# Performance work log

Measured on AMD Instinct MI355X. Metric: run time of the kernel, lower is better.

Reference implementation:

```python
import jax, jax.numpy as jnp
import numpy as np

SC = 30.0
M = 0.5
EPS = 1e-12  # F.normalize default eps


def _l2norm(x, axis):
    n = jnp.sqrt(jnp.sum(x * x, axis=axis, keepdims=True))
    return x / jnp.maximum(n, EPS)


def setup_inputs() -> dict:
    key = jax.random.key(0)
    k1, k2, k3, k4, k5 = jax.random.split(key, 5)
    n, in_f, out_f, books, words = 1024, 2048, 4096, 8, 256
    lw = in_f // books  # len_word = 256
    # xavier_uniform-ish scale for params
    w_lim = np.sqrt(6.0 / (out_f + lw))
    m_lim = np.sqrt(6.0 / (lw + words))
    return {
        "input": jax.random.normal(k1, (n, in_f), dtype=jnp.float32),
        "label": jax.random.randint(k2, (n,), 0, out_f, dtype=jnp.int64),
        "weight": jax.random.uniform(k3, (books, out_f, lw), jnp.float32, -w_lim, w_lim),
        "mlp": jax.random.uniform(k4, (books, lw, words), jnp.float32, -m_lim, m_lim),
        "codebooks": jax.random.normal(k5, (books, lw, words), dtype=jnp.float32),
    }


def reference(input, label, weight, mlp, codebooks):
    n, in_f = input.shape
    books, out_f, lw = weight.shape
    # split input into per-book chunks: [books, n, lw]
    x = input.reshape(n, books, lw).transpose(1, 0, 2)
    wn = _l2norm(weight, axis=2)               # [books, out_f, lw]
    xn = _l2norm(x, axis=2)                    # [books, n, lw]
    cos_xw = jnp.clip(jnp.einsum('bnd,bod->bno', xn, wn), -1.0, 1.0)  # [books,n,out_f]
    # per-book soft codeword assignment
    xc_soft = jax.nn.softmax(jnp.einsum('bnd,bdw->bnw', x, mlp), axis=2)  # [books,n,words]
    # soft-quantized features s_m: codebooks @ xc_soft^T -> [books, lw, n] -> [books, n, lw]
    s = jnp.einsum('bdw,bnw->bnd', codebooks, xc_soft)
    sn = _l2norm(s, axis=2)
    cos_sw = jnp.clip(jnp.einsum('bnd,bod->bno', sn, wn), -1.0, 1.0)
    # margin one-hot combine: oh*(cos - m) + (1-oh)*cos == cos - oh*m
    oh = jax.nn.one_hot(label, out_f, dtype=cos_xw.dtype)[None]  # [1, n, out_f]
    out1 = SC * (cos_xw - oh * M)
    out2 = SC * (cos_sw - oh * M)
    return (out1.transpose(1, 0, 2), out2.transpose(1, 0, 2), xc_soft.transpose(1, 0, 2))
```

## Files before the change

kernel.cpp:

```cpp
#include <hip/hip_runtime.h>

typedef __attribute__((ext_vector_type(8))) short short8;
typedef __attribute__((ext_vector_type(4))) float f32x4;
typedef __attribute__((ext_vector_type(8))) unsigned short u16x8;

#define BOOKS 8
#define NSAMP 1024
#define OUTF  4096
#define KDIM  256
#define OUT2_OFF 33554432ull
#define OUT3_OFF 67108864ull

__device__ __forceinline__ unsigned short f2bf(float f) {
  unsigned int u = __float_as_uint(f);
  u += 0x7fffu + ((u >> 16) & 1u);
  return (unsigned short)(u >> 16);
}
__device__ __forceinline__ float b2f(unsigned short u) {
  return __uint_as_float((unsigned)u << 16);
}

__device__ __forceinline__ float wave_sum(float v) {
  #pragma unroll
  for (int off = 32; off; off >>= 1) v += __shfl_xor(v, off, 64);
  return v;
}
__device__ __forceinline__ float qsum(float v) {
  #pragma unroll
  for (int off = 1; off < 16; off <<= 1) v += __shfl_xor(v, off, 64);
  return v;
}
__device__ __forceinline__ float qmax(float v) {
  #pragma unroll
  for (int off = 1; off < 16; off <<= 1) v = fmaxf(v, __shfl_xor(v, off, 64));
  return v;
}

__device__ __forceinline__ void gll16(const void* g, void* l) {
  __builtin_amdgcn_global_load_lds((const __attribute__((address_space(1))) void*)g,
                                   (__attribute__((address_space(3))) void*)l,
                                   16, 0, 0);
}

__global__ __launch_bounds__(256) void prep_kernel(const float* __restrict__ input,
                                                   const float* __restrict__ weight,
                                                   const float* __restrict__ mlp,
                                                   const float* __restrict__ cb,
                                                   unsigned short* __restrict__ wn,
                                                   unsigned short* __restrict__ Xb,
                                                   unsigned short* __restrict__ An,
                                                   unsigned short* __restrict__ mlpT,
                                                   unsigned short* __restrict__ cbb) {
  __shared__ float lt[64][65];
  const int blk = blockIdx.x;
  const int tid = threadIdx.x;

  if (blk < 8192) {
    int row  = blk * 4 + (tid >> 6);
    int lane = tid & 63;
    float4 v = ((const float4*)(weight + (size_t)row * KDIM))[lane];
    float ss = wave_sum(v.x*v.x + v.y*v.y + v.z*v.z + v.w*v.w);
    float inv = 1.f / fmaxf(sqrtf(ss), 1e-12f);
    ushort4 o;
    o.x = f2bf(v.x*inv); o.y = f2bf(v.y*inv); o.z = f2bf(v.z*inv); o.w = f2bf(v.w*inv);
    *(ushort4*)(wn + (size_t)row * KDIM + lane * 4) = o;
  } else if (blk < 10240) {
    int id = (blk - 8192) * 4 + (tid >> 6);
    int b = id >> 10, i = id & 1023;
    int lane = tid & 63;
    float4 v = ((const float4*)(input + (size_t)i * 2048 + b * 256))[lane];
    float ss = wave_sum(v.x*v.x + v.y*v.y + v.z*v.z + v.w*v.w);
    float inv = 1.f / fmaxf(sqrtf(ss), 1e-12f);
    ushort4 r;
    r.x = f2bf(v.x); r.y = f2bf(v.y); r.z = f2bf(v.z); r.w = f2bf(v.w);
    *(ushort4*)(Xb + (size_t)id * KDIM + lane * 4) = r;
    ushort4 n;
    n.x = f2bf(v.x*inv); n.y = f2bf(v.y*inv); n.z = f2bf(v.z*inv); n.w = f2bf(v.w*inv);
    *(ushort4*)(An + ((size_t)b * 2048 + i) * KDIM + lane * 4) = n;
  } else {
    int t = blk - 10240;
    int b = t >> 4, tile = t & 15;
    int dt = (tile >> 2) * 64, wt = (tile & 3) * 64;
    int g  = tid >> 4;
    int l4 = (tid & 15) * 4;
    const float* mb = mlp + (size_t)b * 256 * 256;
    const float* cs = cb  + (size_t)b * 256 * 256;
    #pragma unroll
    for (int p = 0; p < 4; ++p) {
      int d = dt + p * 16 + g;
      float4 v = *(const float4*)(mb + (size_t)d * 256 + wt + l4);
      lt[p * 16 + g][l4 + 0] = v.x;
      lt[p * 16 + g][l4 + 1] = v.y;
      lt[p * 16 + g][l4 + 2] = v.z;
      lt[p * 16 + g][l4 + 3] = v.w;
      float4 c = *(const float4*)(cs + (size_t)d * 256 + wt + l4);
      ushort4 co;
      co.x = f2bf(c.x); co.y = f2bf(c.y); co.z = f2bf(c.z); co.w = f2bf(c.w);
      *(ushort4*)(cbb + ((size_t)(b * 256 + d)) * 256 + wt + l4) = co;
    }
    __syncthreads();
    #pragma unroll
    for (int p = 0; p < 4; ++p) {
      int w = wt + p * 16 + g;
      ushort4 o;
      o.x = f2bf(lt[l4 + 0][p * 16 + g]);
      o.y = f2bf(lt[l4 + 1][p * 16 + g]);
      o.z = f2bf(lt[l4 + 2][p * 16 + g]);
      o.w = f2bf(lt[l4 + 3][p * 16 + g]);
      *(ushort4*)(mlpT + ((size_t)(b * 256 + w)) * 256 + dt + l4) = o;
    }
  }
}

__global__ __launch_bounds__(256) void mid_kernel(const unsigned short* __restrict__ Xb,
                                                  const unsigned short* __restrict__ mlpT,
                                                  const unsigned short* __restrict__ cbb,
                                                  unsigned short* __restrict__ An,
                                                  float* __restrict__ out3) {
  __shared__ __align__(16) unsigned short lA[64 * 32];
  __shared__ __align__(16) unsigned short lB[256 * 32];
  __shared__ __align__(16) unsigned short lX[64 * 256];

  const int b  = blockIdx.x >> 4;
  const int m0 = (blockIdx.x & 15) * 64;
  const int tid  = threadIdx.x;
  const int wv   = tid >> 6;
  const int lane = tid & 63;
  const int r16  = lane & 15;
  const int q    = lane >> 4;

  const unsigned short* Ab = Xb   + ((size_t)b * NSAMP + m0) * KDIM;
  const unsigned short* Bm = mlpT + (size_t)b * 256 * KDIM;
  const unsigned short* Bc = cbb  + (size_t)b * 256 * KDIM;

  f32x4 acc[16];
  #pragma unroll
  for (int j = 0; j < 16; ++j) acc[j] = (f32x4){0.f, 0.f, 0.f, 0.f};

  for (int k0 = 0; k0 < KDIM; k0 += 32) {
    __syncthreads();
    { int row = tid >> 2, ko = (tid & 3) * 8;
      gll16(Ab + (size_t)row * KDIM + k0 + ko, &lA[tid * 8]); }
    #pragma unroll
    for (int c = 0; c < 4; ++c) {
      int idx = c * 256 + tid;
      int row = idx >> 2, ko = (idx & 3) * 8;
      gll16(Bm + (size_t)row * KDIM + k0 + ko, &lB[idx * 8]);
    }
    __syncthreads();
    short8 af = *(const short8*)(lA + (wv * 16 + r16) * 32 + q * 8);
    #pragma unroll
    for (int j = 0; j < 16; ++j) {
      short8 bf = *(const short8*)(lB + (j * 16 + r16) * 32 + q * 8);
      acc[j] = __builtin_amdgcn_mfma_f32_16x16x32_bf16(af, bf, acc[j], 0, 0, 0);
    }
  }

  #pragma unroll
  for (int r = 0; r < 4; ++r) {
    float mx = acc[0][r];
    #pragma unroll
    for (int j = 1; j < 16; ++j) mx = fmaxf(mx, acc[j][r]);
    mx = qmax(mx);
    float s = 0.f;
    #pragma unroll
    for (int j = 0; j < 16; ++j) { float e = __expf(acc[j][r] - mx); acc[j][r] = e; s += e; }
    s = qsum(s);
    float inv = 1.f / s;
    int row = wv * 16 + q * 4 + r;
    unsigned rb  = (unsigned)row * 512;
    unsigned msk = ((unsigned)(row & 7)) << 4;
    #pragma unroll
    for (int j = 0; j < 16; ++j) {
      unsigned byte = (rb + (unsigned)(j * 16 + r16) * 2) ^ msk;
      *(unsigned short*)((char*)lX + byte) = f2bf(acc[j][r] * inv);
    }
  }
  __syncthreads();

  #pragma unroll
  for (int p = 0; p < 8; ++p) {
    int chunk = p * 256 + tid;
    int row = chunk >> 5;
    int c8  = (chunk & 31) * 8;
    unsigned byte = ((unsigned)(row * 512 + c8 * 2)) ^ (((unsigned)(row & 7)) << 4);
    u16x8 v = *(const u16x8*)((char*)lX + byte);
    size_t o = ((size_t)(m0 + row) * 8 + b) * 256 + c8;
    f32x4 f0 = { b2f(v[0]), b2f(v[1]), b2f(v[2]), b2f(v[3]) };
    f32x4 f1 = { b2f(v[4]), b2f(v[5]), b2f(v[6]), b2f(v[7]) };
    __builtin_nontemporal_store(f0, (f32x4*)(out3 + o));
    __builtin_nontemporal_store(f1, (f32x4*)(out3 + o + 4));
  }

  #pragma unroll
  for (int j = 0; j < 16; ++j) acc[j] = (f32x4){0.f, 0.f, 0.f, 0.f};
  for (int k0 = 0; k0 < KDIM; k0 += 32) {
    __syncthreads();
    #pragma unroll
    for (int c = 0; c < 4; ++c) {
      int idx = c * 256 + tid;
      int row = idx >> 2, ko = (idx & 3) * 8;
      gll16(Bc + (size_t)row * KDIM + k0 + ko, &lB[idx * 8]);
    }
    __syncthreads();
    int arow = wv * 16 + r16;
    unsigned abyte = ((unsigned)(arow * 512 + (k0 + q * 8) * 2)) ^ (((unsigned)(arow & 7)) << 4);
    short8 af = *(const short8*)((char*)lX + abyte);
    #pragma unroll
    for (int j = 0; j < 16; ++j) {
      short8 bf = *(const short8*)(lB + (j * 16 + r16) * 32 + q * 8);
      acc[j] = __builtin_amdgcn_mfma_f32_16x16x32_bf16(af, bf, acc[j], 0, 0, 0);
    }
  }

  #pragma unroll
  for (int r = 0; r < 4; ++r) {
    float ss = 0.f;
    #pragma unroll
    for (int j = 0; j < 16; ++j) ss += acc[j][r] * acc[j][r];
    ss = qsum(ss);
    float iv = 1.f / fmaxf(sqrtf(ss), 1e-12f);
    int row = wv * 16 + q * 4 + r;
    unsigned rb  = (unsigned)row * 512;
    unsigned msk = ((unsigned)(row & 7)) << 4;
    #pragma unroll
    for (int j = 0; j < 16; ++j) {
      unsigned byte = (rb + (unsigned)(j * 16 + r16) * 2) ^ msk;
      *(unsigned short*)((char*)lX + byte) = f2bf(acc[j][r] * iv);
    }
  }
  __syncthreads();
  #pragma unroll
  for (int p = 0; p < 8; ++p) {
    int chunk = p * 256 + tid;
    int row = chunk >> 5;
    int c8  = (chunk & 31) * 8;
    unsigned byte = ((unsigned)(row * 512 + c8 * 2)) ^ (((unsigned)(row & 7)) << 4);
    u16x8 v = *(const u16x8*)((char*)lX + byte);
    *(u16x8*)(An + ((size_t)b * 2048 + 1024 + m0 + row) * KDIM + c8) = v;
  }
}

__global__ __launch_bounds__(256) void big_gemm_kernel(const unsigned short* __restrict__ A,
                                                       const unsigned short* __restrict__ B,
                                                       float* __restrict__ Cf,
                                                       const int* __restrict__ label) {
  __shared__ __align__(16) unsigned short lA[128 * 32];
  __shared__ __align__(16) unsigned short lB[128 * 32];

  const int b  = blockIdx.z;
  const int lin = blockIdx.x + (blockIdx.y << 5);
  const int wg  = ((lin & 7) << 6) + (lin >> 3);
  const int n0 = (wg & 31) * 128;
  const int m0 = (wg >> 5) * 128;
  const int tid  = threadIdx.x;
  const int wid  = tid >> 6;
  const int lane = tid & 63;
  const int wm = wid & 1, wn = wid >> 1;
  const int r16 = lane & 15;
  const int q   = lane >> 4;

  const unsigned short* Ab = A + (size_t)b * 2048 * KDIM;
  const unsigned short* Bb = B + (size_t)b * OUTF * KDIM;

  f32x4 acc[4][4];
  #pragma unroll
  for (int i = 0; i < 4; ++i)
    #pragma unroll
    for (int j = 0; j < 4; ++j) acc[i][j] = (f32x4){0.f, 0.f, 0.f, 0.f};

  for (int k0 = 0; k0 < KDIM; k0 += 32) {
    __syncthreads();
    #pragma unroll
    for (int c = 0; c < 2; ++c) {
      int idx = c * 256 + tid;
      int row = idx >> 2, ko = (idx & 3) * 8;
      gll16(Ab + (size_t)(m0 + row) * KDIM + k0 + ko, &lA[idx * 8]);
      gll16(Bb + (size_t)(n0 + row) * KDIM + k0 + ko, &lB[idx * 8]);
    }
    __syncthreads();

    short8 af[4], bfr[4];
    #pragma unroll
    for (int f = 0; f < 4; ++f) {
      af[f]  = *(const short8*)(lA + (wm * 64 + f * 16 + r16) * 32 + q * 8);
      bfr[f] = *(const short8*)(lB + (wn * 64 + f * 16 + r16) * 32 + q * 8);
    }
    #pragma unroll
    for (int i = 0; i < 4; ++i)
      #pragma unroll
      for (int j = 0; j < 4; ++j)
        acc[i][j] = __builtin_amdgcn_mfma_f32_16x16x32_bf16(af[i], bfr[j], acc[i][j], 0, 0, 0);
  }

  #pragma unroll
  for (int i = 0; i < 4; ++i) {
    int row0 = m0 + wm * 64 + i * 16 + q * 4;
    #pragma unroll
    for (int r = 0; r < 4; ++r) {
      int row = row0 + r;
      int gi  = row & 1023;
      int lb  = label[gi];
      size_t base = (size_t)(row >> 10) * OUT2_OFF + ((size_t)gi * 8 + b) * OUTF;
      #pragma unroll
      for (int j = 0; j < 4; ++j) {
        int col = n0 + wn * 64 + j * 16 + r16;
        float v = fminf(fmaxf(acc[i][j][r], -1.f), 1.f) * 30.f;
        if (col == lb) v -= 15.f;
        __builtin_nontemporal_store(v, &Cf[base + col]);
      }
    }
  }
}

extern "C" void kernel_launch(void* const* d_in, const int* in_sizes, int n_in,
                              void* d_out, int out_size, void* d_ws, size_t ws_size,
                              hipStream_t stream) {
  const float* input  = (const float*)d_in[0];
  const int*   label  = (const int*)d_in[1];
  const float* weight = (const float*)d_in[2];
  const float* mlp    = (const float*)d_in[3];
  const float* cb     = (const float*)d_in[4];
  float* out = (float*)d_out;

  unsigned short* wn = (unsigned short*)d_ws;
  unsigned short* An = wn + 8388608;

  unsigned short* Xb   = (unsigned short*)(out + OUT2_OFF);
  unsigned short* mlpT = Xb + 2097152;
  unsigned short* cbb  = mlpT + 524288;
  float*          out3 = out + OUT3_OFF;

  prep_kernel<<<dim3(10368), dim3(256), 0, stream>>>(input, weight, mlp, cb,
                                                     wn, Xb, An, mlpT, cbb);
  mid_kernel<<<dim3(128), dim3(256), 0, stream>>>(Xb, mlpT, cbb, An, out3);
  big_gemm_kernel<<<dim3(32, 16, 8), dim3(256), 0, stream>>>(An, wn, out, label);
}
```

Before: 373.7 us.

## Split mid_kernel across more blocks with cross-wave row reductions; drop GEMM block swizzle

mid_kernel now uses 256 blocks of 512 threads, each handling 32 rows instead of 64. The 256 output columns are split across four wave groups, so the softmax max/sum and the L2 norm are combined through shared-memory partials with extra barriers. The aim is better occupancy and more CU coverage for a kernel that previously launched only 128 blocks. Separately, the big GEMM drops its XCD-aware block-index swizzle in favour of a direct blockIdx mapping, which may change L2 locality.

```diff
diff --git a/kernel.cpp b/kernel.cpp
--- a/kernel.cpp
+++ b/kernel.cpp
@@ -112,20 +112,25 @@
   }
 }
 
-__global__ __launch_bounds__(256) void mid_kernel(const unsigned short* __restrict__ Xb,
+__global__ __launch_bounds__(512) void mid_kernel(const unsigned short* __restrict__ Xb,
                                                   const unsigned short* __restrict__ mlpT,
                                                   const unsigned short* __restrict__ cbb,
                                                   unsigned short* __restrict__ An,
                                                   float* __restrict__ out3) {
-  __shared__ __align__(16) unsigned short lA[64 * 32];
+  __shared__ __align__(16) unsigned short lA[32 * 32];
   __shared__ __align__(16) unsigned short lB[256 * 32];
-  __shared__ __align__(16) unsigned short lX[64 * 256];
-
-  const int b  = blockIdx.x >> 4;
-  const int m0 = (blockIdx.x & 15) * 64;
+  __shared__ __align__(16) unsigned short lX[32 * 256];
+  __shared__ float smx[32][4];
+  __shared__ float ssm[32][4];
+  __shared__ float sqs[32][4];
+
+  const int b  = blockIdx.x >> 5;
+  const int m0 = (blockIdx.x & 31) * 32;
   const int tid  = threadIdx.x;
-  const int wv   = tid >> 6;
+  const int wid  = tid >> 6;
   const int lane = tid & 63;
+  const int wm = wid & 1;
+  const int wj = wid >> 1;
   const int r16  = lane & 15;
   const int q    = lane >> 4;
 
@@ -133,54 +138,67 @@
   const unsigned short* Bm = mlpT + (size_t)b * 256 * KDIM;
   const unsigned short* Bc = cbb  + (size_t)b * 256 * KDIM;
 
-  f32x4 acc[16];
-  #pragma unroll
-  for (int j = 0; j < 16; ++j) acc[j] = (f32x4){0.f, 0.f, 0.f, 0.f};
+  f32x4 acc[4];
+  #pragma unroll
+  for (int j = 0; j < 4; ++j) acc[j] = (f32x4){0.f, 0.f, 0.f, 0.f};
 
   for (int k0 = 0; k0 < KDIM; k0 += 32) {
     __syncthreads();
-    { int row = tid >> 2, ko = (tid & 3) * 8;
-      gll16(Ab + (size_t)row * KDIM + k0 + ko, &lA[tid * 8]); }
-    #pragma unroll
-    for (int c = 0; c < 4; ++c) {
-      int idx = c * 256 + tid;
+    if (tid < 128) {
+      int row = tid >> 2, ko = (tid & 3) * 8;
+      gll16(Ab + (size_t)row * KDIM + k0 + ko, &lA[tid * 8]);
+    }
+    #pragma unroll
+    for (int c = 0; c < 2; ++c) {
+      int idx = c * 512 + tid;
       int row = idx >> 2, ko = (idx & 3) * 8;
       gll16(Bm + (size_t)row * KDIM + k0 + ko, &lB[idx * 8]);
     }
     __syncthreads();
-    short8 af = *(const short8*)(lA + (wv * 16 + r16) * 32 + q * 8);
-    #pragma unroll
-    for (int j = 0; j < 16; ++j) {
-      short8 bf = *(const short8*)(lB + (j * 16 + r16) * 32 + q * 8);
+    short8 af = *(const short8*)(lA + (wm * 16 + r16) * 32 + q * 8);
+    #pragma unroll
+    for (int j = 0; j < 4; ++j) {
+      short8 bf = *(const short8*)(lB + ((wj * 4 + j) * 16 + r16) * 32 + q * 8);
       acc[j] = __builtin_amdgcn_mfma_f32_16x16x32_bf16(af, bf, acc[j], 0, 0, 0);
     }
   }
 
   #pragma unroll
   for (int r = 0; r < 4; ++r) {
-    float mx = acc[0][r];
-    #pragma unroll
-    for (int j = 1; j < 16; ++j) mx = fmaxf(mx, acc[j][r]);
+    float mx = fmaxf(fmaxf(acc[0][r], acc[1][r]), fmaxf(acc[2][r], acc[3][r]));
     mx = qmax(mx);
+    int rt = wm * 16 + q * 4 + r;
+    if (r16 == 0) smx[rt][wj] = mx;
+  }
+  __syncthreads();
+  #pragma unroll
+  for (int r = 0; r < 4; ++r) {
+    int rt = wm * 16 + q * 4 + r;
+    float mx = fmaxf(fmaxf(smx[rt][0], smx[rt][1]), fmaxf(smx[rt][2], smx[rt][3]));
     float s = 0.f;
     #pragma unroll
-    for (int j = 0; j < 16; ++j) { float e = __expf(acc[j][r] - mx); acc[j][r] = e; s += e; }
+    for (int j = 0; j < 4; ++j) { float e = __expf(acc[j][r] - mx); acc[j][r] = e; s += e; }
     s = qsum(s);
-    float inv = 1.f / s;
-    int row = wv * 16 + q * 4 + r;
-    unsigned rb  = (unsigned)row * 512;
-    unsigned msk = ((unsigned)(row & 7)) << 4;
-    #pragma unroll
-    for (int j = 0; j < 16; ++j) {
-      unsigned byte = (rb + (unsigned)(j * 16 + r16) * 2) ^ msk;
+    if (r16 == 0) ssm[rt][wj] = s;
+  }
+  __syncthreads();
+  #pragma unroll
+  for (int r = 0; r < 4; ++r) {
+    int rt = wm * 16 + q * 4 + r;
+    float inv = 1.f / (ssm[rt][0] + ssm[rt][1] + ssm[rt][2] + ssm[rt][3]);
+    unsigned rb  = (unsigned)rt * 512;
+    unsigned msk = ((unsigned)(rt & 7)) << 4;
+    #pragma unroll
+    for (int j = 0; j < 4; ++j) {
+      unsigned byte = (rb + (unsigned)((wj * 4 + j) * 16 + r16) * 2) ^ msk;
       *(unsigned short*)((char*)lX + byte) = f2bf(acc[j][r] * inv);
     }
   }
   __syncthreads();
 
   #pragma unroll
-  for (int p = 0; p < 8; ++p) {
-    int chunk = p * 256 + tid;
+  for (int p = 0; p < 2; ++p) {
+    int chunk = p * 512 + tid;
     int row = chunk >> 5;
     int c8  = (chunk & 31) * 8;
     unsigned byte = ((unsigned)(row * 512 + c8 * 2)) ^ (((unsigned)(row & 7)) << 4);
@@ -193,22 +211,22 @@
   }
 
   #pragma unroll
-  for (int j = 0; j < 16; ++j) acc[j] = (f32x4){0.f, 0.f, 0.f, 0.f};
+  for (int j = 0; j < 4; ++j) acc[j] = (f32x4){0.f, 0.f, 0.f, 0.f};
   for (int k0 = 0; k0 < KDIM; k0 += 32) {
     __syncthreads();
     #pragma unroll
-    for (int c = 0; c < 4; ++c) {
-      int idx = c * 256 + tid;
+    for (int c = 0; c < 2; ++c) {
+      int idx = c * 512 + tid;
       int row = idx >> 2, ko = (idx & 3) * 8;
       gll16(Bc + (size_t)row * KDIM + k0 + ko, &lB[idx * 8]);
     }
     __syncthreads();
-    int arow = wv * 16 + r16;
+    int arow = wm * 16 + r16;
     unsigned abyte = ((unsigned)(arow * 512 + (k0 + q * 8) * 2)) ^ (((unsigned)(arow & 7)) << 4);
     short8 af = *(const short8*)((char*)lX + abyte);
     #pragma unroll
-    for (int j = 0; j < 16; ++j) {
-      short8 bf = *(const short8*)(lB + (j * 16 + r16) * 32 + q * 8);
+    for (int j = 0; j < 4; ++j) {
+      short8 bf = *(const short8*)(lB + ((wj * 4 + j) * 16 + r16) * 32 + q * 8);
       acc[j] = __builtin_amdgcn_mfma_f32_16x16x32_bf16(af, bf, acc[j], 0, 0, 0);
     }
   }
@@ -217,22 +235,29 @@
   for (int r = 0; r < 4; ++r) {
     float ss = 0.f;
     #pragma unroll
-    for (int j = 0; j < 16; ++j) ss += acc[j][r] * acc[j][r];
+    for (int j = 0; j < 4; ++j) ss += acc[j][r] * acc[j][r];
     ss = qsum(ss);
-    float iv = 1.f / fmaxf(sqrtf(ss), 1e-12f);
-    int row = wv * 16 + q * 4 + r;
-    unsigned rb  = (unsigned)row * 512;
-    unsigned msk = ((unsigned)(row & 7)) << 4;
-    #pragma unroll
-    for (int j = 0; j < 16; ++j) {
-      unsigned byte = (rb + (unsigned)(j * 16 + r16) * 2) ^ msk;
+    int rt = wm * 16 + q * 4 + r;
+    if (r16 == 0) sqs[rt][wj] = ss;
+  }
+  __syncthreads();
+  #pragma unroll
+  for (int r = 0; r < 4; ++r) {
+    int rt = wm * 16 + q * 4 + r;
+    float tot = sqs[rt][0] + sqs[rt][1] + sqs[rt][2] + sqs[rt][3];
+    float iv = 1.f / fmaxf(sqrtf(tot), 1e-12f);
+    unsigned rb  = (unsigned)rt * 512;
+    unsigned msk = ((unsigned)(rt & 7)) << 4;
+    #pragma unroll
+    for (int j = 0; j < 4; ++j) {
+      unsigned byte = (rb + (unsigned)((wj * 4 + j) * 16 + r16) * 2) ^ msk;
       *(unsigned short*)((char*)lX + byte) = f2bf(acc[j][r] * iv);
     }
   }
   __syncthreads();
   #pragma unroll
-  for (int p = 0; p < 8; ++p) {
-    int chunk = p * 256 + tid;
+  for (int p = 0; p < 2; ++p) {
+    int chunk = p * 512 + tid;
     int row = chunk >> 5;
     int c8  = (chunk & 31) * 8;
     unsigned byte = ((unsigned)(row * 512 + c8 * 2)) ^ (((unsigned)(row & 7)) << 4);
@@ -249,10 +274,8 @@
   __shared__ __align__(16) unsigned short lB[128 * 32];
 
   const int b  = blockIdx.z;
-  const int lin = blockIdx.x + (blockIdx.y << 5);
-  const int wg  = ((lin & 7) << 6) + (lin >> 3);
-  const int n0 = (wg & 31) * 128;
-  const int m0 = (wg >> 5) * 128;
+  const int n0 = blockIdx.x * 128;
+  const int m0 = blockIdx.y * 128;
   const int tid  = threadIdx.x;
   const int wid  = tid >> 6;
   const int lane = tid & 63;
@@ -333,6 +356,6 @@
 
   prep_kernel<<<dim3(10368), dim3(256), 0, stream>>>(input, weight, mlp, cb,
                                                      wn, Xb, An, mlpT, cbb);
-  mid_kernel<<<dim3(128), dim3(256), 0, stream>>>(Xb, mlpT, cbb, An, out3);
+  mid_kernel<<<dim3(256), dim3(512), 0, stream>>>(Xb, mlpT, cbb, An, out3);
   big_gemm_kernel<<<dim3(32, 16, 8), dim3(256), 0, stream>>>(An, wn, out, label);
 }
```

Result: faster. 365.2 us (-2.3%).
